# Kernel tuning notes

Measured on AMD Instinct MI355X. Metric: run time of the kernel, lower is better.

The kernel has to match this reference:

```python
import jax, jax.numpy as jnp
import numpy as np

IN_CH = (512, 1024, 512, 256, 256, 256)
CORR = 9          # patch_size of spatial_correlation_sample
UP = 1            # upsample_param
BASE = 96         # level-0 spatial size
B = 2
NEG_SLOPE = 0.01  # nn.LeakyReLU default


def _upsample_nearest(x, s):
    # nearest upsample by integer factor s (matches nn.Upsample(mode='nearest'))
    if s == 1:
        return x
    return jnp.repeat(jnp.repeat(x, s, axis=2), s, axis=3)


def _downsample_nearest(x, s):
    # nearest 'upsample' with scale 1/s: out[d] = in[d*s]
    if s == 1:
        return x
    return x[:, :, ::s, ::s]


def _spatial_correlation(f1, f2, patch):
    # kernel_size=1, stride=1, padding=0, dilation_patch=1, zero pad for
    # out-of-bounds displacements. Returns [b, patch*patch, h, w]
    r = patch // 2
    b, c, h, w = f1.shape
    f2p = jnp.pad(f2, ((0, 0), (0, 0), (r, r), (r, r)))
    vols = [jnp.einsum('bchw,bchw->bhw', f1, f2p[:, :, di:di + h, dj:dj + w])
            for di in range(patch) for dj in range(patch)]
    return jnp.stack(vols, axis=1)


def _forward(xs, xps):
    outs = []
    for i, (feat1, feat2) in enumerate(zip(xs, xps)):
        s = UP * (2 ** i)
        up1 = _upsample_nearest(feat1, s)
        up2 = _upsample_nearest(feat2, s)
        corr = _spatial_correlation(up1, up2, CORR)          # [b, 81, H, W]
        corr = jnp.where(corr >= 0, corr, NEG_SLOPE * corr)  # LeakyReLU
        dw = _downsample_nearest(corr, s)
        dw = dw / jnp.max(dw)                                # global max-normalize
        outs += [dw, corr]
    return tuple(outs)  # flattened list of (dw_corr_feat, corr_feat) pairs


def setup_inputs() -> dict:
    key = jax.random.key(0)
    ks = jax.random.split(key, 12)
    sizes = [BASE // (2 ** i) for i in range(6)]
    inp = {}
    for i in range(6):
        shp = (B, IN_CH[i], sizes[i], sizes[i])
        inp[f'x{i}'] = jax.random.normal(ks[i], shp, dtype=jnp.float32)
        inp[f'xp{i}'] = jax.random.normal(ks[6 + i], shp, dtype=jnp.float32)
    inp['motion_state'] = jnp.zeros((6,), dtype=jnp.float32)  # consumed by zip, never read
    return inp


def reference(x0, x1, x2, x3, x4, x5, xp0, xp1, xp2, xp3, xp4, xp5, motion_state):
    return _forward((x0, x1, x2, x3, x4, x5), (xp0, xp1, xp2, xp3, xp4, xp5))
```

## Files before the change

kernel.cpp:

```cpp
#include <hip/hip_runtime.h>
#include <hip/hip_bf16.h>

#define CEIL(a, b) (((a) + (b) - 1) / (b))

typedef __hip_bfloat16 bf16;
typedef __attribute__((ext_vector_type(2))) _Float16 h16x2;


__global__ __launch_bounds__(64) void k_corr0s(
    const float* __restrict__ f1, const float* __restrict__ f2,
    bf16* __restrict__ part) {
  const int l = threadIdx.x;
  const int xt = blockIdx.x;
  const int y = blockIdx.y;
  const int gc = blockIdx.z >> 1;
  const int b = blockIdx.z & 1;
  const int x0 = xt * 48;

  float acc[9][9];
#pragma unroll
  for (int j = 0; j < 9; ++j)
#pragma unroll
    for (int i = 0; i < 9; ++i) acc[j][i] = 0.f;

  const int xa = x0 - 4 + l;
  const bool ok_a = (l < 56) && (xa >= 0) && (xa < 96);
  const int aoff = y * 96 + (xa < 0 ? 0 : (xa > 95 ? 95 : xa));
  const int xv = x0 + (l < 48 ? l : 47);
  bool okv[9];
  int voff[9];
#pragma unroll
  for (int t = 0; t < 9; ++t) {
    int yy = y - 4 + t;
    okv[t] = (l < 48) && (yy >= 0) && (yy < 96);
    voff[t] = (yy < 0 ? 0 : (yy > 95 ? 95 : yy)) * 96 + xv;
  }

  const float* f1b = f1 + (size_t)b * 512 * 9216;
  const float* f2b = f2 + (size_t)b * 512 * 9216;
  const int c0 = gc * 64;
  for (int c = c0; c < c0 + 64; c += 2) {
    float a0 = f1b[(size_t)c * 9216 + aoff];
    float a1 = f1b[(size_t)(c + 1) * 9216 + aoff];
    unsigned au =
        __builtin_bit_cast(unsigned, __builtin_amdgcn_cvt_pkrtz(a0, a1));
    au = ok_a ? au : 0u;
    unsigned asu[9];
#pragma unroll
    for (int i = 0; i < 9; ++i)
      asu[i] = (i == 8) ? au : (unsigned)__shfl((int)au, l + 8 - i);
    unsigned vus[9];
#pragma unroll
    for (int t = 0; t < 9; ++t) {
      float v0 = f2b[(size_t)c * 9216 + voff[t]];
      float v1 = f2b[(size_t)(c + 1) * 9216 + voff[t]];
      unsigned vu =
          __builtin_bit_cast(unsigned, __builtin_amdgcn_cvt_pkrtz(v0, v1));
      vus[t] = okv[t] ? vu : 0u;
    }
#pragma unroll
    for (int j = 0; j < 9; ++j) {
      h16x2 vp = __builtin_bit_cast(h16x2, vus[j]);
#pragma unroll
      for (int i = 0; i < 9; ++i)
        acc[j][i] = __builtin_amdgcn_fdot2(
            __builtin_bit_cast(h16x2, asu[i]), vp, acc[j][i], false);
    }
  }

  if (l < 48) {
    size_t base = ((size_t)((gc * 2 + b) * 96 + y)) * 7776 + x0 + l;
#pragma unroll
    for (int j = 0; j < 9; ++j)
#pragma unroll
      for (int i = 0; i < 9; ++i)
        part[base + (size_t)(j * 9 + i) * 96] = __float2bfloat16(acc[j][i]);
  }
}

__global__ __launch_bounds__(256) void k_corr0red(
    const bf16* __restrict__ part, float* __restrict__ corr0,
    float* __restrict__ maxbuf) {
  const int t = blockIdx.x * 256 + threadIdx.x;
  const int x = t % 96;
  const int y = (t / 96) % 96;
  const int d = (t / 9216) % 81;
  const int b = t / 746496;
  const int dx = d % 9;
  const int xs = x + dx - 4;
  float v = 0.f;
  if (xs >= 0 && xs < 96) {
    size_t base = ((size_t)(b * 96 + y)) * 7776 + (size_t)d * 96 + xs;
    const size_t gstride = (size_t)2 * 96 * 7776;
#pragma unroll
    for (int gc = 0; gc < 8; ++gc)
      v += __bfloat162float(part[base + gc * gstride]);
  }
  v = v >= 0.f ? v : 0.01f * v;
  corr0[t] = v;
  float mx = v;
#pragma unroll
  for (int off = 32; off; off >>= 1) mx = fmaxf(mx, __shfl_down(mx, off));
  __shared__ float wm[4];
  if ((threadIdx.x & 63) == 0) wm[threadIdx.x >> 6] = mx;
  __syncthreads();
  if (threadIdx.x == 0)
    maxbuf[blockIdx.x] = fmaxf(fmaxf(wm[0], wm[1]), fmaxf(wm[2], wm[3]));
}

__global__ __launch_bounds__(64) void k_lc1p(
    const float* __restrict__ f1, const float* __restrict__ f2,
    float* __restrict__ part) {
  const int X = threadIdx.x;
  const int Y = blockIdx.x;
  const int gc = blockIdx.y;
  const int b = blockIdx.z;
  const bool xin = (X < 48);

  float acc2[5][5];
#pragma unroll
  for (int i = 0; i < 5; ++i)
#pragma unroll
    for (int j = 0; j < 5; ++j) acc2[i][j] = 0.f;

  bool okdy[5];
  int voff[5];
#pragma unroll
  for (int dy = 0; dy < 5; ++dy) {
    int YY = Y + dy - 2;
    okdy[dy] = (YY >= 0 && YY < 48) && xin;
    voff[dy] = (YY < 0 ? 0 : (YY > 47 ? 47 : YY)) * 48 + (xin ? X : 0);
  }
  const float* p1 = f1 + (size_t)b * 1024 * 2304 + Y * 48;
  const float* p2 = f2 + (size_t)b * 1024 * 2304;

  const int c0 = gc * 32;
#pragma unroll 2
  for (int c = c0; c < c0 + 32; c += 2) {
    float a0 = xin ? p1[(size_t)c * 2304 + X] : 0.f;
    float a1 = xin ? p1[(size_t)(c + 1) * 2304 + X] : 0.f;
    unsigned au =
        __builtin_bit_cast(unsigned, __builtin_amdgcn_cvt_pkrtz(a0, a1));
    unsigned asu[5];
#pragma unroll
    for (int dx = 0; dx < 5; ++dx) {
      int src = X - dx + 2;
      src = src < 0 ? 0 : (src > 63 ? 63 : src);
      asu[dx] = (dx == 2) ? au : (unsigned)__shfl((int)au, src);
    }
#pragma unroll
    for (int dy = 0; dy < 5; ++dy) {
      float v0 = p2[(size_t)c * 2304 + voff[dy]];
      float v1 = p2[(size_t)(c + 1) * 2304 + voff[dy]];
      unsigned vu =
          __builtin_bit_cast(unsigned, __builtin_amdgcn_cvt_pkrtz(v0, v1));
      vu = okdy[dy] ? vu : 0u;
      h16x2 vp = __builtin_bit_cast(h16x2, vu);
#pragma unroll
      for (int dx = 0; dx < 5; ++dx)
        acc2[dy][dx] = __builtin_amdgcn_fdot2(
            __builtin_bit_cast(h16x2, asu[dx]), vp, acc2[dy][dx], false);
    }
  }

  float* pb = part + ((size_t)(gc * 2 + b) * 25) * 2304 + Y * 48;
#pragma unroll
  for (int dy = 0; dy < 5; ++dy)
#pragma unroll
    for (int dx = 0; dx < 5; ++dx) {
      int src = X + dx - 2;
      int scl = src < 0 ? 0 : (src > 63 ? 63 : src);
      float val = __shfl(acc2[dy][dx], scl);
      bool okx = (X + dx - 2 >= 0) && (X + dx - 2 < 48);
      bool oky = (Y + dy - 2 >= 0) && (Y + dy - 2 < 48);
      if (xin)
        pb[(size_t)(dy * 5 + dx) * 2304 + X] = (oky && okx) ? val : 0.f;
    }
}

__global__ __launch_bounds__(64) void k_lcrow_all(
    const float* __restrict__ x2, const float* __restrict__ q2,
    const float* __restrict__ x3, const float* __restrict__ q3,
    const float* __restrict__ x4, const float* __restrict__ q4,
    const float* __restrict__ x5, const float* __restrict__ q5,
    float* __restrict__ out) {
  int bx = blockIdx.x;
  int S, C, RW;
  const float *f1, *f2;
  float* part;
  if (bx < 12) {
    S = 24; C = 512; RW = 2; f1 = x2; f2 = q2; part = out + 200000;
  } else if (bx < 15) {
    bx -= 12; S = 12; C = 256; RW = 5; f1 = x3; f2 = q3; part = out + 600000;
  } else if (bx < 16) {
    bx -= 15; S = 6; C = 256; RW = 10; f1 = x4; f2 = q4; part = out + 700000;
  } else {
    bx -= 16; S = 3; C = 256; RW = 21; f1 = x5; f2 = q5; part = out + 730000;
  }
  const int cpg = C / 32;
  const int lane = threadIdx.x;
  const int SS = S * S;
  const int yr = lane / S;
  const int X = lane % S;
  const int y = bx * RW + yr;
  const int gc = blockIdx.y;
  const int b = blockIdx.z;
  const bool act = (yr < RW) && (y < S);

  float acc[3][3];
#pragma unroll
  for (int i = 0; i < 3; ++i)
#pragma unroll
    for (int j = 0; j < 3; ++j) acc[i][j] = 0.f;

  bool okdx[3], okdy[3];
  int off1[3], off2[3];
#pragma unroll
  for (int i = 0; i < 3; ++i) {
    int xs = X + 1 - i;
    okdx[i] = act && (xs >= 0) && (xs < S);
    off1[i] = (act ? y : 0) * S + (xs < 0 ? 0 : (xs >= S ? S - 1 : xs));
    int yy = y + i - 1;
    okdy[i] = act && (yy >= 0) && (yy < S);
    off2[i] = (yy < 0 ? 0 : (yy >= S ? S - 1 : yy)) * S + X;
  }

  const float* f1b = f1 + (size_t)b * C * SS;
  const float* f2b = f2 + (size_t)b * C * SS;
  const int c0 = gc * cpg;
  for (int c = c0; c < c0 + cpg; c += 2) {
    const float* p = f1b + (size_t)c * SS;
    const float* pn = p + SS;
    const float* q = f2b + (size_t)c * SS;
    const float* qn = q + SS;
    unsigned au[3], vu[3];
#pragma unroll
    for (int i = 0; i < 3; ++i) {
      unsigned u = __builtin_bit_cast(
          unsigned, __builtin_amdgcn_cvt_pkrtz(p[off1[i]], pn[off1[i]]));
      au[i] = okdx[i] ? u : 0u;
      unsigned w = __builtin_bit_cast(
          unsigned, __builtin_amdgcn_cvt_pkrtz(q[off2[i]], qn[off2[i]]));
      vu[i] = okdy[i] ? w : 0u;
    }
#pragma unroll
    for (int dy = 0; dy < 3; ++dy) {
      h16x2 vp = __builtin_bit_cast(h16x2, vu[dy]);
#pragma unroll
      for (int dxi = 0; dxi < 3; ++dxi)
        acc[dy][dxi] = __builtin_amdgcn_fdot2(
            __builtin_bit_cast(h16x2, au[dxi]), vp, acc[dy][dxi], false);
    }
  }

  if (act) {
    size_t base = ((size_t)(gc * 2 + b) * S + y) * 9 * S + X;
#pragma unroll
    for (int dy = 0; dy < 3; ++dy)
#pragma unroll
      for (int dxi = 0; dxi < 3; ++dxi)
        part[base + (size_t)(dy * 3 + dxi) * S] = acc[dy][dxi];
  }
}

__global__ __launch_bounds__(256) void k_red_all(float* __restrict__ out) {
  int t = blockIdx.x * 256 + threadIdx.x;
  if (t < 115200) {
    const float* part = out + 3359232;
    const int o = t / 4608;
    const int pix = t % 4608;
    const int b = pix / 2304, r = pix % 2304;
    float s = 0.f;
#pragma unroll
    for (int g = 0; g < 32; ++g)
      s += part[((size_t)(g * 2 + b) * 25 + o) * 2304 + r];
    out[(size_t)pix * 25 + o] = s;
    return;
  }
  t -= 115200;
  int S;
  const float* part;
  float* lc;
  if (t < 10368) {
    S = 24; part = out + 200000; lc = out + 115200;
  } else if ((t -= 10368) < 2592) {
    S = 12; part = out + 600000; lc = out + 125568;
  } else if ((t -= 2592) < 648) {
    S = 6; part = out + 700000; lc = out + 128160;
  } else if ((t -= 648) < 162) {
    S = 3; part = out + 730000; lc = out + 128808;
  } else {
    return;
  }
  const int SS = S * S;
  const int o = t % 9;
  const int p = t / 9;
  const int b = p / SS, r = p % SS, y = r / S, X = r % S;
  const int dy = o / 3, dx = o % 3;
  const int xs = X + dx - 1;
  float v = 0.f;
  if (xs >= 0 && xs < S) {
    size_t base = ((size_t)b * S + y) * 9 * S + (size_t)(dy * 3 + dx) * S + xs;
    const size_t gstride = (size_t)2 * S * 9 * S;
#pragma unroll
    for (int g = 0; g < 32; ++g) v += part[base + g * gstride];
  }
  lc[(size_t)p * 9 + o] = v;
}

__global__ __launch_bounds__(256) void k_expand_all(
    float* __restrict__ out, float* __restrict__ maxbuf) {
  static const int lcoffs[6] = {0, 0, 115200, 125568, 128160, 128808};
  static const size_t dwo[6] = {0,       2985984, 4852224,
                                6438528, 7954848, 9453672};
  static const size_t cro[6] = {1492992, 3359232, 4945536,
                                6461856, 7960680, 9455130};
  const int lvl = (int)blockIdx.y + 1;
  const int R = (lvl == 1) ? 2 : 1;
  const float* lc = out + lcoffs[lvl];
  float* out_corr = out + cro[lvl];
  float* out_dw = out + dwo[lvl];
  const int t = blockIdx.x * 256 + threadIdx.x;
  float contrib = 0.f;
  {
    const int x = t % 96;
    const int y = (t / 96) % 96;
    const int d = (t / 9216) % 81;
    const int b = t / 746496;
    const int hy = y + d / 9 - 4;
    const int hx = x + d % 9 - 4;
    float val = 0.f;
    if (hy >= 0 && hy < 96 && hx >= 0 && hx < 96) {
      const int S = 96 >> lvl;
      const int Y1 = y >> lvl, X1 = x >> lvl;
      const int oy = (hy >> lvl) - Y1 + R;
      const int ox = (hx >> lvl) - X1 + R;
      const int DD = 2 * R + 1;
      val = lc[(((size_t)(b * S + Y1) * S + X1) * DD + oy) * DD + ox];
      val = val >= 0.f ? val : 0.01f * val;
    }
    out_corr[t] = val;
    const int m = (1 << lvl) - 1;
    if (((y | x) & m) == 0) {
      const int S = 96 >> lvl;
      out_dw[((size_t)(b * 81 + d) * S + (y >> lvl)) * S + (x >> lvl)] = val;
      contrib = val;
    }
  }
#pragma unroll
  for (int off = 32; off; off >>= 1)
    contrib = fmaxf(contrib, __shfl_down(contrib, off));
  __shared__ float wm[4];
  if ((threadIdx.x & 63) == 0) wm[threadIdx.x >> 6] = contrib;
  __syncthreads();
  if (threadIdx.x == 0)
    maxbuf[(size_t)lvl * 5832 + blockIdx.x] =
        fmaxf(fmaxf(wm[0], wm[1]), fmaxf(wm[2], wm[3]));
}

__global__ __launch_bounds__(1024) void k_finmax(
    const float* __restrict__ maxbuf, unsigned int* __restrict__ slots) {
  const int lvl = blockIdx.x;
  const float* mb = maxbuf + (size_t)lvl * 5832;
  float m = 0.f;
  for (int i = threadIdx.x; i < 5832; i += 1024) m = fmaxf(m, mb[i]);
#pragma unroll
  for (int off = 32; off; off >>= 1) m = fmaxf(m, __shfl_down(m, off));
  __shared__ float wm[16];
  if ((threadIdx.x & 63) == 0) wm[threadIdx.x >> 6] = m;
  __syncthreads();
  if (threadIdx.x == 0) {
    float r = wm[0];
#pragma unroll
    for (int i = 1; i < 16; ++i) r = fmaxf(r, wm[i]);
    slots[lvl] = (unsigned int)__float_as_int(r);
  }
}

__global__ __launch_bounds__(256) void k_norm_all(
    float* __restrict__ out, const unsigned int* __restrict__ slots) {
  int i = blockIdx.x * 256 + threadIdx.x;
  int lvl;
  size_t dst, src;
  if (i < 1492986) {
    lvl = 0; dst = i; src = (size_t)1492992 + i;
  } else if ((i -= 1492986) < 373248) {
    lvl = 1; dst = (size_t)2985984 + i; src = dst;
  } else if ((i -= 373248) < 93312) {
    lvl = 2; dst = (size_t)4852224 + i; src = dst;
  } else if ((i -= 93312) < 23328) {
    lvl = 3; dst = (size_t)6438528 + i; src = dst;
  } else if ((i -= 23328) < 5832) {
    lvl = 4; dst = (size_t)7954848 + i; src = dst;
  } else if ((i -= 5832) < 1458) {
    lvl = 5; dst = (size_t)9453672 + i; src = dst;
  } else {
    return;
  }
  const float m = __int_as_float((int)slots[lvl]);
  out[dst] = out[src] / m;
}

__global__ __launch_bounds__(64) void k_norm0_tail(
    float* __restrict__ out, const unsigned int* __restrict__ slots) {
  const float m = __int_as_float((int)slots[0]);
  if (threadIdx.x < 6) {
    const int t = 1492986 + threadIdx.x;
    out[t] = out[1492992 + t] / m;
  }
}

extern "C" void kernel_launch(void* const* d_in, const int* in_sizes, int n_in,
                              void* d_out, int out_size, void* d_ws,
                              size_t ws_size, hipStream_t stream) {
  const float* x[6];
  const float* xp[6];
  for (int i = 0; i < 6; ++i) {
    x[i] = (const float*)d_in[2 * i];
    xp[i] = (const float*)d_in[2 * i + 1];
  }
  float* out = (float*)d_out;

  float* maxbuf = out + 1400000;
  unsigned int* slots = (unsigned int*)(out + 1492986);
  bf16* part0 = (bf16*)(out + 2985984);
  float* part1 = out + 3359232;

  const int NORM_TOTAL = 1492986 + 373248 + 93312 + 23328 + 5832 + 1458;

  k_corr0s<<<dim3(2, 96, 16), dim3(64), 0, stream>>>(x[0], xp[0], part0);
  k_corr0red<<<dim3(5832), dim3(256), 0, stream>>>(part0, out + 1492992,
                                                   maxbuf);
  k_lc1p<<<dim3(48, 32, 2), dim3(64), 0, stream>>>(x[1], xp[1], part1);
  k_lcrow_all<<<dim3(17, 32, 2), dim3(64), 0, stream>>>(
      x[2], xp[2], x[3], xp[3], x[4], xp[4], x[5], xp[5], out);
  k_red_all<<<dim3(CEIL(128970, 256)), dim3(256), 0, stream>>>(out);
  k_expand_all<<<dim3(5832, 5), dim3(256), 0, stream>>>(out, maxbuf);
  k_finmax<<<dim3(6), dim3(1024), 0, stream>>>(maxbuf, slots);
  k_norm_all<<<dim3(CEIL(NORM_TOTAL, 256)), dim3(256), 0, stream>>>(out,
                                                                    slots);
  k_norm0_tail<<<dim3(1), dim3(64), 0, stream>>>(out, slots);
}
```

Baseline: 119.8 us.

## Fuse level-0 correlation partial sums and reduction into one LDS-atomic kernel

The level-0 correlation used to write bf16 partial sums per channel group to global memory, then reduce them in a second kernel. Now one 1024-thread block per (row, batch) puts the 8 channel-group waves together, accumulates shifted results into an LDS buffer with shared atomics, and applies LeakyReLU, the store and the per-block max directly. This removes the partial-buffer round trip and one launch. In exchange it launches only 192 large blocks, which may underfill the GPU, and adds LDS atomic contention. It also sums in fp32 instead of through bf16 partials.

Result: slower. 287.0 us (+139.5%).

```diff
diff --git a/kernel.cpp b/kernel.cpp
--- a/kernel.cpp
+++ b/kernel.cpp
@@ -7,15 +7,22 @@
 typedef __attribute__((ext_vector_type(2))) _Float16 h16x2;
 
 
-__global__ __launch_bounds__(64) void k_corr0s(
+__global__ __launch_bounds__(1024) void k_corr0f(
     const float* __restrict__ f1, const float* __restrict__ f2,
-    bf16* __restrict__ part) {
-  const int l = threadIdx.x;
-  const int xt = blockIdx.x;
-  const int y = blockIdx.y;
-  const int gc = blockIdx.z >> 1;
-  const int b = blockIdx.z & 1;
-  const int x0 = xt * 48;
+    float* __restrict__ corr0, float* __restrict__ maxbuf) {
+  __shared__ float lds[81 * 96];
+  __shared__ float wmx[16];
+  const int tid = threadIdx.x;
+  const int l = tid & 63;
+  const int wid = tid >> 6;
+  const int xh = wid & 1;
+  const int gc = wid >> 1;
+  const int y = blockIdx.x;
+  const int b = blockIdx.y;
+  const int x0 = xh * 48;
+
+  for (int i = tid; i < 7776; i += 1024) lds[i] = 0.f;
+  __syncthreads();
 
   float acc[9][9];
 #pragma unroll
@@ -69,43 +76,35 @@
   }
 
   if (l < 48) {
-    size_t base = ((size_t)((gc * 2 + b) * 96 + y)) * 7776 + x0 + l;
 #pragma unroll
     for (int j = 0; j < 9; ++j)
 #pragma unroll
-      for (int i = 0; i < 9; ++i)
-        part[base + (size_t)(j * 9 + i) * 96] = __float2bfloat16(acc[j][i]);
-  }
-}
-
-__global__ __launch_bounds__(256) void k_corr0red(
-    const bf16* __restrict__ part, float* __restrict__ corr0,
-    float* __restrict__ maxbuf) {
-  const int t = blockIdx.x * 256 + threadIdx.x;
-  const int x = t % 96;
-  const int y = (t / 96) % 96;
-  const int d = (t / 9216) % 81;
-  const int b = t / 746496;
-  const int dx = d % 9;
-  const int xs = x + dx - 4;
-  float v = 0.f;
-  if (xs >= 0 && xs < 96) {
-    size_t base = ((size_t)(b * 96 + y)) * 7776 + (size_t)d * 96 + xs;
-    const size_t gstride = (size_t)2 * 96 * 7776;
-#pragma unroll
-    for (int gc = 0; gc < 8; ++gc)
-      v += __bfloat162float(part[base + gc * gstride]);
-  }
-  v = v >= 0.f ? v : 0.01f * v;
-  corr0[t] = v;
-  float mx = v;
+      for (int i = 0; i < 9; ++i) {
+        int xo = x0 + l + 4 - i;
+        if (xo >= 0 && xo < 96)
+          atomicAdd(&lds[(j * 9 + i) * 96 + xo], acc[j][i]);
+      }
+  }
+  __syncthreads();
+
+  float mx = 0.f;
+  for (int s = tid; s < 7776; s += 1024) {
+    float v = lds[s];
+    v = v >= 0.f ? v : 0.01f * v;
+    mx = fmaxf(mx, v);
+    int d = s / 96, x = s % 96;
+    corr0[(size_t)(b * 81 + d) * 9216 + y * 96 + x] = v;
+  }
 #pragma unroll
   for (int off = 32; off; off >>= 1) mx = fmaxf(mx, __shfl_down(mx, off));
-  __shared__ float wm[4];
-  if ((threadIdx.x & 63) == 0) wm[threadIdx.x >> 6] = mx;
+  if (l == 0) wmx[wid] = mx;
   __syncthreads();
-  if (threadIdx.x == 0)
-    maxbuf[blockIdx.x] = fmaxf(fmaxf(wm[0], wm[1]), fmaxf(wm[2], wm[3]));
+  if (tid == 0) {
+    float r = wmx[0];
+#pragma unroll
+    for (int i = 1; i < 16; ++i) r = fmaxf(r, wmx[i]);
+    maxbuf[y * 2 + b] = r;
+  }
 }
 
 __global__ __launch_bounds__(64) void k_lc1p(
@@ -361,9 +360,10 @@
 __global__ __launch_bounds__(1024) void k_finmax(
     const float* __restrict__ maxbuf, unsigned int* __restrict__ slots) {
   const int lvl = blockIdx.x;
+  const int n = (lvl == 0) ? 192 : 5832;
   const float* mb = maxbuf + (size_t)lvl * 5832;
   float m = 0.f;
-  for (int i = threadIdx.x; i < 5832; i += 1024) m = fmaxf(m, mb[i]);
+  for (int i = threadIdx.x; i < n; i += 1024) m = fmaxf(m, mb[i]);
 #pragma unroll
   for (int off = 32; off; off >>= 1) m = fmaxf(m, __shfl_down(m, off));
   __shared__ float wm[16];
@@ -423,14 +423,12 @@
 
   float* maxbuf = out + 1400000;
   unsigned int* slots = (unsigned int*)(out + 1492986);
-  bf16* part0 = (bf16*)(out + 2985984);
   float* part1 = out + 3359232;
 
   const int NORM_TOTAL = 1492986 + 373248 + 93312 + 23328 + 5832 + 1458;
 
-  k_corr0s<<<dim3(2, 96, 16), dim3(64), 0, stream>>>(x[0], xp[0], part0);
-  k_corr0red<<<dim3(5832), dim3(256), 0, stream>>>(part0, out + 1492992,
-                                                   maxbuf);
+  k_corr0f<<<dim3(96, 2), dim3(1024), 0, stream>>>(x[0], xp[0],
+                                                   out + 1492992, maxbuf);
   k_lc1p<<<dim3(48, 32, 2), dim3(64), 0, stream>>>(x[1], xp[1], part1);
   k_lcrow_all<<<dim3(17, 32, 2), dim3(64), 0, stream>>>(
       x[2], xp[2], x[3], xp[3], x[4], xp[4], x[5], xp[5], out);
```
